# Kernel tuning notes

Measured on AMD Instinct MI355X. Metric: run time of the kernel, lower is better.

The kernel has to match this reference:

```python
import jax, jax.numpy as jnp
import numpy as np

D_MODEL = 384
D_INNER = 768   # 2 * d_model
D_STATE = 16
DT_RANK = 24    # ceil(d_model/16)
K_CONV = 4
BATCH = 8
SEQ = 2048
EPS = 1e-5


def _layer_norm(x, w, b):
    mu = x.mean(-1, keepdims=True)
    var = ((x - mu) ** 2).mean(-1, keepdims=True)
    return (x - mu) * jax.lax.rsqrt(var + EPS) * w + b


def _silu(x):
    return x * jax.nn.sigmoid(x)


def _mamba_mixer(x, in_proj, conv_w, conv_b, x_proj, dt_w, dt_b, A_log, Dp, out_proj):
    # x: (B, L, d_model)
    xz = x @ in_proj.T                      # (B, L, 2*d_inner)
    xs, z = jnp.split(xz, 2, axis=-1)       # each (B, L, d_inner)
    # causal depthwise conv1d (pad left k-1)
    xc = jnp.transpose(xs, (0, 2, 1))       # (B, d_inner, L)
    xc = jnp.pad(xc, ((0, 0), (0, 0), (K_CONV - 1, 0)))
    xc = jax.lax.conv_general_dilated(
        xc, conv_w, window_strides=(1,), padding='VALID',
        feature_group_count=D_INNER,
        dimension_numbers=('NCH', 'OIH', 'NCH'))
    xs = _silu(jnp.transpose(xc, (0, 2, 1)) + conv_b)   # (B, L, d_inner)
    # input-dependent SSM parameters
    x_dbl = xs @ x_proj.T                    # (B, L, dt_rank + 2*d_state)
    dt, Bm, Cm = jnp.split(x_dbl, [DT_RANK, DT_RANK + D_STATE], axis=-1)
    dt = jax.nn.softplus(dt @ dt_w.T + dt_b)  # (B, L, d_inner)
    A = -jnp.exp(A_log)                       # (d_inner, d_state)

    def step(h, inp):
        dt_t, B_t, C_t, x_t = inp             # (B,d), (B,N), (B,N), (B,d)
        h = jnp.exp(dt_t[:, :, None] * A) * h + (dt_t * x_t)[:, :, None] * B_t[:, None, :]
        y = jnp.einsum('bdn,bn->bd', h, C_t)
        return h, y

    h0 = jnp.zeros((xs.shape[0], D_INNER, D_STATE), xs.dtype)
    inps = (jnp.moveaxis(dt, 1, 0), jnp.moveaxis(Bm, 1, 0),
            jnp.moveaxis(Cm, 1, 0), jnp.moveaxis(xs, 1, 0))
    _, ys = jax.lax.scan(step, h0, inps)      # ys: (L, B, d_inner)
    y = jnp.moveaxis(ys, 0, 1) + xs * Dp      # skip term D*x
    y = y * _silu(z)                          # gated output
    return y @ out_proj.T                     # (B, L, d_model)


def setup_inputs() -> dict:
    key = jax.random.key(0)
    ks = jax.random.split(key, 10)
    s = 0.02
    A_init = jnp.broadcast_to(jnp.log(jnp.arange(1, D_STATE + 1, dtype=jnp.float32)),
                              (2, D_INNER, D_STATE))
    return {
        'x': jax.random.normal(ks[0], (BATCH, SEQ, D_MODEL), jnp.float32),
        'norm_w': jnp.ones((2, D_MODEL), jnp.float32),
        'norm_b': jnp.zeros((2, D_MODEL), jnp.float32),
        'in_proj': jax.random.normal(ks[1], (2, 2 * D_INNER, D_MODEL)) * s,
        'conv_w': jax.random.normal(ks[2], (2, D_INNER, 1, K_CONV)) * 0.2,
        'conv_b': jax.random.normal(ks[3], (2, D_INNER)) * s,
        'x_proj': jax.random.normal(ks[4], (2, DT_RANK + 2 * D_STATE, D_INNER)) * s,
        'dt_w': jax.random.normal(ks[5], (2, D_INNER, DT_RANK)) * s,
        'dt_b': jax.random.normal(ks[6], (2, D_INNER)) * 0.1 - 4.0,
        'A_log': A_init,
        'Dp': jnp.ones((2, D_INNER), jnp.float32),
        'out_proj': jax.random.normal(ks[7], (2, D_MODEL, D_INNER)) * s,
    }


def reference(x, norm_w, norm_b, in_proj, conv_w, conv_b, x_proj, dt_w, dt_b, A_log, Dp, out_proj):
    def blk(i, h):
        return h + _mamba_mixer(_layer_norm(h, norm_w[i], norm_b[i]),
                                in_proj[i], conv_w[i], conv_b[i], x_proj[i],
                                dt_w[i], dt_b[i], A_log[i], Dp[i], out_proj[i])
    h = blk(0, x)                    # forward-direction block
    h = jnp.flip(h, axis=-2)         # reverse sequence
    h = blk(1, h)                    # backward-direction block
    return jnp.flip(h, axis=-2)      # restore order
```

## Files before the change

### kernel.cpp

```cpp
#include <hip/hip_runtime.h>
#include <hip/hip_bf16.h>
#include <cstddef>

#define D_MODEL 384
#define D_INNER 768
#define D_STATE 16
#define DT_RANK 24
#define K_CONV  4
#define BATCH   8
#define SEQ     2048
#define BL      (BATCH * SEQ)
#define NCHUNK  32
#define LCHUNK  (SEQ / NCHUNK)
#define XDBL_LD 64

typedef unsigned short ushort_t;
typedef __bf16 bf16x8 __attribute__((ext_vector_type(8)));
typedef float  f32x4  __attribute__((ext_vector_type(4)));
typedef unsigned short u16x8 __attribute__((ext_vector_type(8)));

#define GLOBAL_AS(p) ((const __attribute__((address_space(1))) void*)(p))
#define LDS_AS(p)    ((__attribute__((address_space(3))) void*)(p))

__device__ __forceinline__ ushort_t f32_to_bf16_rne(float v) {
    unsigned int u = __float_as_uint(v);
    return (ushort_t)((u + 0x7FFFu + ((u >> 16) & 1u)) >> 16);
}
__device__ __forceinline__ float bf16_to_f32(ushort_t u) {
    return __uint_as_float(((unsigned int)u) << 16);
}

__global__ __launch_bounds__(256) void cast_bf16_kernel(
    const float* __restrict__ in, ushort_t* __restrict__ out, int n)
{
    int i = blockIdx.x * 256 + threadIdx.x;
    if (i < n) out[i] = f32_to_bf16_rne(in[i]);
}

__global__ __launch_bounds__(256) void cast_xproj_kernel(
    const float* __restrict__ in, ushort_t* __restrict__ out)
{
    int i = blockIdx.x * 256 + threadIdx.x;
    if (i >= 2 * 64 * D_INNER) return;
    int c   = i % D_INNER;
    int r   = (i / D_INNER) % 64;
    int dir = i / (64 * D_INNER);
    out[i] = (r < 56) ? f32_to_bf16_rne(in[((size_t)dir * 56 + r) * D_INNER + c])
                      : (ushort_t)0;
}

__global__ __launch_bounds__(256) void prep_transpose_kernel(
    const float* __restrict__ conv_w, const float* __restrict__ A_log,
    const float* __restrict__ dt_w, float* __restrict__ cwt,
    float* __restrict__ alt, float* __restrict__ dwt)
{
    int i = blockIdx.x * 256 + threadIdx.x;
    const int NCW = 2 * K_CONV * D_INNER;
    const int NAL = 2 * D_STATE * D_INNER;
    const int NDW = 2 * DT_RANK * D_INNER;
    if (i < NCW) {
        int c = i % D_INNER, k = (i / D_INNER) % K_CONV, dir = i / (K_CONV * D_INNER);
        cwt[i] = conv_w[((size_t)dir * D_INNER + c) * K_CONV + k];
    } else if (i < NCW + NAL) {
        int j = i - NCW;
        int d = j % D_INNER, n = (j / D_INNER) % D_STATE, dir = j / (D_STATE * D_INNER);
        alt[j] = A_log[((size_t)dir * D_INNER + d) * D_STATE + n];
    } else if (i < NCW + NAL + NDW) {
        int j = i - NCW - NAL;
        int d = j % D_INNER, r = (j / D_INNER) % DT_RANK, dir = j / (DT_RANK * D_INNER);
        dwt[j] = dt_w[((size_t)dir * D_INNER + d) * DT_RANK + r];
    }
}

__global__ __launch_bounds__(384) void ln_kernel(
    const float* __restrict__ in, const float* __restrict__ w,
    const float* __restrict__ b, ushort_t* __restrict__ out)
{
    int row = blockIdx.x;
    int tid = threadIdx.x;
    float v = in[(size_t)row * D_MODEL + tid];
    float s = v, sq = v * v;
    #pragma unroll
    for (int o = 32; o; o >>= 1) {
        s  += __shfl_down(s, o);
        sq += __shfl_down(sq, o);
    }
    __shared__ float ss[6], ssq[6];
    __shared__ float mb[2];
    int wid = tid >> 6;
    if ((tid & 63) == 0) { ss[wid] = s; ssq[wid] = sq; }
    __syncthreads();
    if (tid == 0) {
        float S = 0.f, Q = 0.f;
        #pragma unroll
        for (int k = 0; k < 6; k++) { S += ss[k]; Q += ssq[k]; }
        float mu  = S * (1.0f / D_MODEL);
        float var = Q * (1.0f / D_MODEL) - mu * mu;
        mb[0] = mu;
        mb[1] = rsqrtf(var + 1e-5f);
    }
    __syncthreads();
    float r = (v - mb[0]) * mb[1] * w[tid] + b[tid];
    out[(size_t)row * D_MODEL + tid] = f32_to_bf16_rne(r);
}

__global__ __launch_bounds__(256) void gemm_mfma_b16(
    const ushort_t* __restrict__ A, const ushort_t* __restrict__ W,
    ushort_t* __restrict__ C, int N, int K)
{
    __shared__ __bf16 As[128 * 32];
    __shared__ __bf16 Ws[128 * 32];
    int tid  = threadIdx.x;
    int bm = blockIdx.x, bn = blockIdx.y;
    int lane = tid & 63, wave = tid >> 6;
    int wr = wave >> 1, wc = wave & 1;
    int quad = lane >> 4, l16 = lane & 15;

    const ushort_t* Ag = A + (size_t)(bm * 128 + (tid >> 2)) * K + (tid & 3) * 8;
    const ushort_t* Wg = W + (size_t)(bn * 128 + (tid >> 2)) * K + (tid & 3) * 8;

    f32x4 acc[4][4] = {};

    for (int k0 = 0; k0 < K; k0 += 32) {
        __syncthreads();
        __builtin_amdgcn_global_load_lds(GLOBAL_AS(Ag + k0),
                                         LDS_AS(As + tid * 8), 16, 0, 0);
        __builtin_amdgcn_global_load_lds(GLOBAL_AS(Ag + (size_t)64 * K + k0),
                                         LDS_AS(As + 2048 + tid * 8), 16, 0, 0);
        __builtin_amdgcn_global_load_lds(GLOBAL_AS(Wg + k0),
                                         LDS_AS(Ws + tid * 8), 16, 0, 0);
        __builtin_amdgcn_global_load_lds(GLOBAL_AS(Wg + (size_t)64 * K + k0),
                                         LDS_AS(Ws + 2048 + tid * 8), 16, 0, 0);
        __syncthreads();

        bf16x8 af[4], wf[4];
        #pragma unroll
        for (int i = 0; i < 4; i++)
            af[i] = *(const bf16x8*)(As + (wr * 64 + i * 16 + l16) * 32 + quad * 8);
        #pragma unroll
        for (int j = 0; j < 4; j++)
            wf[j] = *(const bf16x8*)(Ws + (wc * 64 + j * 16 + l16) * 32 + quad * 8);
        #pragma unroll
        for (int i = 0; i < 4; i++)
            #pragma unroll
            for (int j = 0; j < 4; j++)
                acc[i][j] = __builtin_amdgcn_mfma_f32_16x16x32_bf16(
                    af[i], wf[j], acc[i][j], 0, 0, 0);
    }

    #pragma unroll
    for (int i = 0; i < 4; i++) {
        #pragma unroll
        for (int r = 0; r < 4; r++) {
            int row = bm * 128 + wr * 64 + i * 16 + quad * 4 + r;
            #pragma unroll
            for (int j = 0; j < 4; j++) {
                int col = bn * 128 + wc * 64 + j * 16 + l16;
                C[(size_t)row * N + col] = f32_to_bf16_rne(acc[i][j][r]);
            }
        }
    }
}

__global__ __launch_bounds__(256) void gemm_mfma_f32(
    const ushort_t* __restrict__ A, const ushort_t* __restrict__ W,
    const float* __restrict__ resid, float* __restrict__ C, int N, int K)
{
    __shared__ __bf16 As[128 * 32];
    __shared__ __bf16 Ws[128 * 32];
    int tid  = threadIdx.x;
    int bm = blockIdx.x, bn = blockIdx.y;
    int lane = tid & 63, wave = tid >> 6;
    int wr = wave >> 1, wc = wave & 1;
    int quad = lane >> 4, l16 = lane & 15;

    const ushort_t* Ag = A + (size_t)(bm * 128 + (tid >> 2)) * K + (tid & 3) * 8;
    const ushort_t* Wg = W + (size_t)(bn * 128 + (tid >> 2)) * K + (tid & 3) * 8;

    f32x4 acc[4][4] = {};

    for (int k0 = 0; k0 < K; k0 += 32) {
        __syncthreads();
        __builtin_amdgcn_global_load_lds(GLOBAL_AS(Ag + k0),
                                         LDS_AS(As + tid * 8), 16, 0, 0);
        __builtin_amdgcn_global_load_lds(GLOBAL_AS(Ag + (size_t)64 * K + k0),
                                         LDS_AS(As + 2048 + tid * 8), 16, 0, 0);
        __builtin_amdgcn_global_load_lds(GLOBAL_AS(Wg + k0),
                                         LDS_AS(Ws + tid * 8), 16, 0, 0);
        __builtin_amdgcn_global_load_lds(GLOBAL_AS(Wg + (size_t)64 * K + k0),
                                         LDS_AS(Ws + 2048 + tid * 8), 16, 0, 0);
        __syncthreads();

        bf16x8 af[4], wf[4];
        #pragma unroll
        for (int i = 0; i < 4; i++)
            af[i] = *(const bf16x8*)(As + (wr * 64 + i * 16 + l16) * 32 + quad * 8);
        #pragma unroll
        for (int j = 0; j < 4; j++)
            wf[j] = *(const bf16x8*)(Ws + (wc * 64 + j * 16 + l16) * 32 + quad * 8);
        #pragma unroll
        for (int i = 0; i < 4; i++)
            #pragma unroll
            for (int j = 0; j < 4; j++)
                acc[i][j] = __builtin_amdgcn_mfma_f32_16x16x32_bf16(
                    af[i], wf[j], acc[i][j], 0, 0, 0);
    }

    #pragma unroll
    for (int i = 0; i < 4; i++) {
        #pragma unroll
        for (int r = 0; r < 4; r++) {
            int row = bm * 128 + wr * 64 + i * 16 + quad * 4 + r;
            #pragma unroll
            for (int j = 0; j < 4; j++) {
                int col = bn * 128 + wc * 64 + j * 16 + l16;
                size_t idx = (size_t)row * N + col;
                C[idx] = acc[i][j][r] + resid[idx];
            }
        }
    }
}

__global__ __launch_bounds__(256) void xdbl_mfma(
    const ushort_t* __restrict__ A, const ushort_t* __restrict__ W,
    float* __restrict__ C)
{
    __shared__ __bf16 As[128 * 32];
    __shared__ __bf16 Ws[64 * 32];
    int tid  = threadIdx.x;
    int bm = blockIdx.x;
    int lane = tid & 63, wave = tid >> 6;
    int quad = lane >> 4, l16 = lane & 15;

    const ushort_t* Ag = A + (size_t)(bm * 128 + (tid >> 2)) * D_INNER + (tid & 3) * 8;
    const ushort_t* Wg = W + (size_t)(tid >> 2) * D_INNER + (tid & 3) * 8;

    f32x4 acc[2][4] = {};

    for (int k0 = 0; k0 < D_INNER; k0 += 32) {
        __syncthreads();
        __builtin_amdgcn_global_load_lds(GLOBAL_AS(Ag + k0),
                                         LDS_AS(As + tid * 8), 16, 0, 0);
        __builtin_amdgcn_global_load_lds(GLOBAL_AS(Ag + (size_t)64 * D_INNER + k0),
                                         LDS_AS(As + 2048 + tid * 8), 16, 0, 0);
        __builtin_amdgcn_global_load_lds(GLOBAL_AS(Wg + k0),
                                         LDS_AS(Ws + tid * 8), 16, 0, 0);
        __syncthreads();

        bf16x8 af[2], wf[4];
        #pragma unroll
        for (int i = 0; i < 2; i++)
            af[i] = *(const bf16x8*)(As + (wave * 32 + i * 16 + l16) * 32 + quad * 8);
        #pragma unroll
        for (int j = 0; j < 4; j++)
            wf[j] = *(const bf16x8*)(Ws + (j * 16 + l16) * 32 + quad * 8);
        #pragma unroll
        for (int i = 0; i < 2; i++)
            #pragma unroll
            for (int j = 0; j < 4; j++)
                acc[i][j] = __builtin_amdgcn_mfma_f32_16x16x32_bf16(
                    af[i], wf[j], acc[i][j], 0, 0, 0);
    }

    #pragma unroll
    for (int i = 0; i < 2; i++) {
        #pragma unroll
        for (int r = 0; r < 4; r++) {
            int row = bm * 128 + wave * 32 + i * 16 + quad * 4 + r;
            #pragma unroll
            for (int j = 0; j < 4; j++) {
                int col = j * 16 + l16;
                C[(size_t)row * XDBL_LD + col] = acc[i][j][r];
            }
        }
    }
}

__global__ __launch_bounds__(256) void conv_silu_kernel(
    const ushort_t* __restrict__ xz, const float* __restrict__ cwt,
    const float* __restrict__ cb, ushort_t* __restrict__ xsc, int dir)
{
    int idx8 = blockIdx.x * 256 + threadIdx.x;
    int c8   = (idx8 % 96) * 8;
    int row  = idx8 / 96;
    int l    = row % SEQ;
    int b0   = row - l;

    float acc[8];
    float4 bv0 = *(const float4*)(cb + c8);
    float4 bv1 = *(const float4*)(cb + c8 + 4);
    acc[0] = bv0.x; acc[1] = bv0.y; acc[2] = bv0.z; acc[3] = bv0.w;
    acc[4] = bv1.x; acc[5] = bv1.y; acc[6] = bv1.z; acc[7] = bv1.w;

    #pragma unroll
    for (int k = 0; k < 4; k++) {
        int ls = dir ? (l + k) : (l - 3 + k);
        int wk = dir ? (3 - k) : k;
        bool ok = dir ? (ls < SEQ) : (ls >= 0);
        if (ok) {
            u16x8 v = *(const u16x8*)(xz + (size_t)(b0 + ls) * 1536 + c8);
            float4 w0 = *(const float4*)(cwt + wk * D_INNER + c8);
            float4 w1 = *(const float4*)(cwt + wk * D_INNER + c8 + 4);
            float wv[8] = {w0.x, w0.y, w0.z, w0.w, w1.x, w1.y, w1.z, w1.w};
            #pragma unroll
            for (int j = 0; j < 8; j++)
                acc[j] = fmaf(bf16_to_f32(v[j]), wv[j], acc[j]);
        }
    }
    u16x8 o;
    #pragma unroll
    for (int j = 0; j < 8; j++) {
        float sg = 1.0f / (1.0f + __expf(-acc[j]));
        o[j] = f32_to_bf16_rne(acc[j] * sg);
    }
    *(u16x8*)(xsc + (size_t)row * D_INNER + c8) = o;
}

__global__ __launch_bounds__(256) void scan_pass1(
    const ushort_t* __restrict__ xsc, const float* __restrict__ xdbl,
    const float* __restrict__ dwt, const float* __restrict__ dtbias,
    const float* __restrict__ alt,
    float* __restrict__ hstate, float* __restrict__ sumdt_buf, int dir)
{
    int g = blockIdx.x % 3;
    int c = (blockIdx.x / 3) % NCHUNK;
    int b = blockIdx.x / (3 * NCHUNK);
    int d = g * 256 + threadIdx.x;
    float A[D_STATE], w[DT_RANK];
    #pragma unroll
    for (int n = 0; n < D_STATE; n++) A[n] = -__expf(alt[n * D_INNER + d]);
    #pragma unroll
    for (int r = 0; r < DT_RANK; r++) w[r] = dwt[r * D_INNER + d];
    float bias = dtbias[d];
    float h[D_STATE] = {};
    float sdt = 0.f;
    size_t base = (size_t)b * SEQ;
    for (int i = 0; i < LCHUNK; i++) {
        int p = c * LCHUNK + i;
        int l = dir ? (SEQ - 1 - p) : p;
        size_t row = base + l;
        const float* xr = xdbl + row * XDBL_LD;
        float acc = bias;
        #pragma unroll
        for (int r = 0; r < DT_RANK; r++) acc = fmaf(xr[r], w[r], acc);
        float dtv = acc > 20.f ? acc : __logf(1.f + __expf(acc));
        float xv  = bf16_to_f32(xsc[row * D_INNER + d]);
        float dtx = dtv * xv;
        sdt += dtv;
        const float* Br = xr + DT_RANK;
        #pragma unroll
        for (int n = 0; n < D_STATE; n++)
            h[n] = fmaf(__expf(dtv * A[n]), h[n], dtx * Br[n]);
    }
    size_t cidx = (size_t)(b * NCHUNK + c) * D_INNER + d;
    sumdt_buf[cidx] = sdt;
    #pragma unroll
    for (int n = 0; n < D_STATE; n++) hstate[cidx * D_STATE + n] = h[n];
}

__global__ __launch_bounds__(256) void scan_pass2(
    float* __restrict__ hstate, const float* __restrict__ sumdt_buf,
    const float* __restrict__ alt)
{
    int gid = blockIdx.x * 256 + threadIdx.x;
    int n = gid & 15;
    int d = (gid >> 4) % D_INNER;
    int b = gid / (16 * D_INNER);
    float A = -__expf(alt[n * D_INNER + d]);
    float h = 0.f;
    for (int c = 0; c < NCHUNK; c++) {
        size_t cidx = (size_t)(b * NCHUNK + c) * D_INNER + d;
        float ho = hstate[cidx * D_STATE + n];
        hstate[cidx * D_STATE + n] = h;
        h = fmaf(__expf(A * sumdt_buf[cidx]), h, ho);
    }
}

__global__ __launch_bounds__(256) void scan_pass3(
    const ushort_t* __restrict__ xsc, const ushort_t* __restrict__ xz,
    const float* __restrict__ xdbl, const float* __restrict__ dwt,
    const float* __restrict__ dtbias, const float* __restrict__ alt,
    const float* __restrict__ Dp, const float* __restrict__ hstate,
    ushort_t* __restrict__ y, int dir)
{
    int g = blockIdx.x % 3;
    int c = (blockIdx.x / 3) % NCHUNK;
    int b = blockIdx.x / (3 * NCHUNK);
    int d = g * 256 + threadIdx.x;
    size_t cidx = (size_t)(b * NCHUNK + c) * D_INNER + d;
    float A[D_STATE], h[D_STATE], w[DT_RANK];
    #pragma unroll
    for (int n = 0; n < D_STATE; n++) {
        A[n] = -__expf(alt[n * D_INNER + d]);
        h[n] = hstate[cidx * D_STATE + n];
    }
    #pragma unroll
    for (int r = 0; r < DT_RANK; r++) w[r] = dwt[r * D_INNER + d];
    float bias = dtbias[d];
    float Dd = Dp[d];
    size_t base = (size_t)b * SEQ;
    for (int i = 0; i < LCHUNK; i++) {
        int p = c * LCHUNK + i;
        int l = dir ? (SEQ - 1 - p) : p;
        size_t row = base + l;
        const float* xr = xdbl + row * XDBL_LD;
        float acc = bias;
        #pragma unroll
        for (int r = 0; r < DT_RANK; r++) acc = fmaf(xr[r], w[r], acc);
        float dtv = acc > 20.f ? acc : __logf(1.f + __expf(acc));
        float xv  = bf16_to_f32(xsc[row * D_INNER + d]);
        float zv  = bf16_to_f32(xz[row * 1536 + D_INNER + d]);
        float dtx = dtv * xv;
        const float* Br = xr + DT_RANK;
        const float* Cr = xr + DT_RANK + D_STATE;
        float yv = 0.f;
        #pragma unroll
        for (int n = 0; n < D_STATE; n++) {
            h[n] = fmaf(__expf(dtv * A[n]), h[n], dtx * Br[n]);
            yv = fmaf(h[n], Cr[n], yv);
        }
        yv = fmaf(xv, Dd, yv);
        float sg = 1.f / (1.f + __expf(-zv));
        yv *= zv * sg;
        y[row * D_INNER + d] = f32_to_bf16_rne(yv);
    }
}

extern "C" void kernel_launch(void* const* d_in, const int* in_sizes, int n_in,
                              void* d_out, int out_size, void* d_ws, size_t ws_size,
                              hipStream_t stream)
{
    const float* x       = (const float*)d_in[0];
    const float* norm_w  = (const float*)d_in[1];
    const float* norm_b  = (const float*)d_in[2];
    const float* in_proj = (const float*)d_in[3];
    const float* conv_w  = (const float*)d_in[4];
    const float* conv_b  = (const float*)d_in[5];
    const float* x_proj  = (const float*)d_in[6];
    const float* dt_w    = (const float*)d_in[7];
    const float* dt_b    = (const float*)d_in[8];
    const float* A_log   = (const float*)d_in[9];
    const float* Dp      = (const float*)d_in[10];
    const float* out_proj= (const float*)d_in[11];
    float* out = (float*)d_out;

    float* ws   = (float*)d_ws;
    float* reg0 = ws;                ws += (size_t)BL * D_INNER / 2;
    ushort_t* lnb = (ushort_t*)reg0;
    ushort_t* ybf = (ushort_t*)reg0;
    ushort_t* xzb  = (ushort_t*)ws;  ws += (size_t)BL * 1536 / 2;
    ushort_t* xscb = (ushort_t*)ws;  ws += (size_t)BL * D_INNER / 2;
    float* xdbl = ws;                ws += (size_t)BL * XDBL_LD;
    float* sumdt  = ws;              ws += (size_t)BATCH * NCHUNK * D_INNER;
    float* hstate = ws;              ws += (size_t)BATCH * NCHUNK * D_INNER * D_STATE;
    ushort_t* wbf_in  = (ushort_t*)ws;  ws += (size_t)2 * 1536 * D_MODEL / 2;
    ushort_t* wbf_out = (ushort_t*)ws;  ws += (size_t)2 * D_MODEL * D_INNER / 2;
    ushort_t* xp_bf   = (ushort_t*)ws;  ws += (size_t)2 * 64 * D_INNER / 2;
    float* cwt = ws;                 ws += (size_t)2 * K_CONV * D_INNER;
    float* alt = ws;                 ws += (size_t)2 * D_STATE * D_INNER;
    float* dwt = ws;                 ws += (size_t)2 * DT_RANK * D_INNER;

    cast_bf16_kernel<<<(2 * 1536 * D_MODEL + 255) / 256, 256, 0, stream>>>(
        in_proj, wbf_in, 2 * 1536 * D_MODEL);
    cast_bf16_kernel<<<(2 * D_MODEL * D_INNER + 255) / 256, 256, 0, stream>>>(
        out_proj, wbf_out, 2 * D_MODEL * D_INNER);
    cast_xproj_kernel<<<(2 * 64 * D_INNER + 255) / 256, 256, 0, stream>>>(
        x_proj, xp_bf);
    {
        int total = 2 * (K_CONV + D_STATE + DT_RANK) * D_INNER;
        prep_transpose_kernel<<<(total + 255) / 256, 256, 0, stream>>>(
            conv_w, A_log, dt_w, cwt, alt, dwt);
    }

    for (int i = 0; i < 2; i++) {
        const float* hinp = (i == 0) ? x : out;
        ln_kernel<<<BL, 384, 0, stream>>>(hinp, norm_w + i * D_MODEL,
                                          norm_b + i * D_MODEL, lnb);
        gemm_mfma_b16<<<dim3(BL / 128, 1536 / 128), 256, 0, stream>>>(
            lnb, wbf_in + (size_t)i * 1536 * D_MODEL, xzb, 1536, D_MODEL);
        conv_silu_kernel<<<(BL * 96) / 256, 256, 0, stream>>>(
            xzb, cwt + (size_t)i * K_CONV * D_INNER, conv_b + i * D_INNER,
            xscb, i);
        xdbl_mfma<<<BL / 128, 256, 0, stream>>>(
            xscb, xp_bf + (size_t)i * 64 * D_INNER, xdbl);
        scan_pass1<<<BATCH * NCHUNK * 3, 256, 0, stream>>>(
            xscb, xdbl, dwt + (size_t)i * DT_RANK * D_INNER,
            dt_b + i * D_INNER, alt + (size_t)i * D_STATE * D_INNER,
            hstate, sumdt, i);
        scan_pass2<<<(BATCH * D_INNER * D_STATE) / 256, 256, 0, stream>>>(
            hstate, sumdt, alt + (size_t)i * D_STATE * D_INNER);
        scan_pass3<<<BATCH * NCHUNK * 3, 256, 0, stream>>>(
            xscb, xzb, xdbl, dwt + (size_t)i * DT_RANK * D_INNER,
            dt_b + i * D_INNER, alt + (size_t)i * D_STATE * D_INNER,
            Dp + i * D_INNER, hstate, ybf, i);
        gemm_mfma_f32<<<dim3(BL / 128, D_MODEL / 128), 256, 0, stream>>>(
            ybf, wbf_out + (size_t)i * D_MODEL * D_INNER, hinp, out,
            D_MODEL, D_INNER);
    }
}
```

Baseline: 594.0 us.

## Precompute dt in separate kernel, double scan chunks, use exp2 with prescaled A

Moves the dt projection and softplus out of both scan passes into a new dt_kernel that writes dt as bf16, so the delta computation runs once instead of twice per direction. Doubles NCHUNK to 64 so the scan passes launch more blocks, and replaces __expf with hardware exp2 by prescaling A with log2(e). The cost is an extra kernel launch, an extra bf16 buffer of BL*D_INNER written and read twice, reduced dt precision from storing it as bf16, and a longer sequential loop in pass2.

Result: faster. 545.7 us (-8.1%).

```diff
diff --git a/kernel.cpp b/kernel.cpp
--- a/kernel.cpp
+++ b/kernel.cpp
@@ -10,9 +10,10 @@
 #define BATCH   8
 #define SEQ     2048
 #define BL      (BATCH * SEQ)
-#define NCHUNK  32
+#define NCHUNK  64
 #define LCHUNK  (SEQ / NCHUNK)
 #define XDBL_LD 64
+#define LOG2E   1.44269504088896f
 
 typedef unsigned short ushort_t;
 typedef __bf16 bf16x8 __attribute__((ext_vector_type(8)));
@@ -276,6 +277,34 @@
     }
 }
 
+__global__ __launch_bounds__(256) void dt_kernel(
+    const float* __restrict__ xdbl, const float* __restrict__ dwt,
+    const float* __restrict__ dtbias, ushort_t* __restrict__ dtb)
+{
+    int g    = blockIdx.x % 3;
+    int row0 = (blockIdx.x / 3) * 16;
+    int tid  = threadIdx.x;
+    int d    = g * 256 + tid;
+    float w[DT_RANK];
+    #pragma unroll
+    for (int r = 0; r < DT_RANK; r++) w[r] = dwt[r * D_INNER + d];
+    float bias = dtbias[d];
+    __shared__ float xd[16][DT_RANK];
+    if (tid < 16 * DT_RANK) {
+        int rr = tid / DT_RANK, cc = tid % DT_RANK;
+        xd[rr][cc] = xdbl[(size_t)(row0 + rr) * XDBL_LD + cc];
+    }
+    __syncthreads();
+    #pragma unroll 4
+    for (int i = 0; i < 16; i++) {
+        float acc = bias;
+        #pragma unroll
+        for (int r = 0; r < DT_RANK; r++) acc = fmaf(xd[i][r], w[r], acc);
+        float sp = acc > 20.f ? acc : __logf(1.f + __expf(acc));
+        dtb[(size_t)(row0 + i) * D_INNER + d] = f32_to_bf16_rne(sp);
+    }
+}
+
 __global__ __launch_bounds__(256) void conv_silu_kernel(
     const ushort_t* __restrict__ xz, const float* __restrict__ cwt,
     const float* __restrict__ cb, ushort_t* __restrict__ xsc, int dir)
@@ -317,21 +346,18 @@
 }
 
 __global__ __launch_bounds__(256) void scan_pass1(
-    const ushort_t* __restrict__ xsc, const float* __restrict__ xdbl,
-    const float* __restrict__ dwt, const float* __restrict__ dtbias,
-    const float* __restrict__ alt,
+    const ushort_t* __restrict__ xsc, const ushort_t* __restrict__ dtb,
+    const float* __restrict__ xdbl, const float* __restrict__ alt,
     float* __restrict__ hstate, float* __restrict__ sumdt_buf, int dir)
 {
     int g = blockIdx.x % 3;
     int c = (blockIdx.x / 3) % NCHUNK;
     int b = blockIdx.x / (3 * NCHUNK);
     int d = g * 256 + threadIdx.x;
-    float A[D_STATE], w[DT_RANK];
-    #pragma unroll
-    for (int n = 0; n < D_STATE; n++) A[n] = -__expf(alt[n * D_INNER + d]);
-    #pragma unroll
-    for (int r = 0; r < DT_RANK; r++) w[r] = dwt[r * D_INNER + d];
-    float bias = dtbias[d];
+    float A2[D_STATE];
+    #pragma unroll
+    for (int n = 0; n < D_STATE; n++)
+        A2[n] = -__expf(alt[n * D_INNER + d]) * LOG2E;
     float h[D_STATE] = {};
     float sdt = 0.f;
     size_t base = (size_t)b * SEQ;
@@ -339,18 +365,14 @@
         int p = c * LCHUNK + i;
         int l = dir ? (SEQ - 1 - p) : p;
         size_t row = base + l;
-        const float* xr = xdbl + row * XDBL_LD;
-        float acc = bias;
-        #pragma unroll
-        for (int r = 0; r < DT_RANK; r++) acc = fmaf(xr[r], w[r], acc);
-        float dtv = acc > 20.f ? acc : __logf(1.f + __expf(acc));
+        float dtv = bf16_to_f32(dtb[row * D_INNER + d]);
         float xv  = bf16_to_f32(xsc[row * D_INNER + d]);
         float dtx = dtv * xv;
         sdt += dtv;
-        const float* Br = xr + DT_RANK;
+        const float* Br = xdbl + row * XDBL_LD + DT_RANK;
         #pragma unroll
         for (int n = 0; n < D_STATE; n++)
-            h[n] = fmaf(__expf(dtv * A[n]), h[n], dtx * Br[n]);
+            h[n] = fmaf(__builtin_amdgcn_exp2f(dtv * A2[n]), h[n], dtx * Br[n]);
     }
     size_t cidx = (size_t)(b * NCHUNK + c) * D_INNER + d;
     sumdt_buf[cidx] = sdt;
@@ -366,57 +388,49 @@
     int n = gid & 15;
     int d = (gid >> 4) % D_INNER;
     int b = gid / (16 * D_INNER);
-    float A = -__expf(alt[n * D_INNER + d]);
+    float A2 = -__expf(alt[n * D_INNER + d]) * LOG2E;
     float h = 0.f;
     for (int c = 0; c < NCHUNK; c++) {
         size_t cidx = (size_t)(b * NCHUNK + c) * D_INNER + d;
         float ho = hstate[cidx * D_STATE + n];
         hstate[cidx * D_STATE + n] = h;
-        h = fmaf(__expf(A * sumdt_buf[cidx]), h, ho);
+        h = fmaf(__builtin_amdgcn_exp2f(A2 * sumdt_buf[cidx]), h, ho);
     }
 }
 
 __global__ __launch_bounds__(256) void scan_pass3(
-    const ushort_t* __restrict__ xsc, const ushort_t* __restrict__ xz,
-    const float* __restrict__ xdbl, const float* __restrict__ dwt,
-    const float* __restrict__ dtbias, const float* __restrict__ alt,
-    const float* __restrict__ Dp, const float* __restrict__ hstate,
-    ushort_t* __restrict__ y, int dir)
+    const ushort_t* __restrict__ xsc, const ushort_t* __restrict__ dtb,
+    const ushort_t* __restrict__ xz, const float* __restrict__ xdbl,
+    const float* __restrict__ alt, const float* __restrict__ Dp,
+    const float* __restrict__ hstate, ushort_t* __restrict__ y, int dir)
 {
     int g = blockIdx.x % 3;
     int c = (blockIdx.x / 3) % NCHUNK;
     int b = blockIdx.x / (3 * NCHUNK);
     int d = g * 256 + threadIdx.x;
     size_t cidx = (size_t)(b * NCHUNK + c) * D_INNER + d;
-    float A[D_STATE], h[D_STATE], w[DT_RANK];
+    float A2[D_STATE], h[D_STATE];
     #pragma unroll
     for (int n = 0; n < D_STATE; n++) {
-        A[n] = -__expf(alt[n * D_INNER + d]);
+        A2[n] = -__expf(alt[n * D_INNER + d]) * LOG2E;
         h[n] = hstate[cidx * D_STATE + n];
     }
-    #pragma unroll
-    for (int r = 0; r < DT_RANK; r++) w[r] = dwt[r * D_INNER + d];
-    float bias = dtbias[d];
     float Dd = Dp[d];
     size_t base = (size_t)b * SEQ;
     for (int i = 0; i < LCHUNK; i++) {
         int p = c * LCHUNK + i;
         int l = dir ? (SEQ - 1 - p) : p;
         size_t row = base + l;
-        const float* xr = xdbl + row * XDBL_LD;
-        float acc = bias;
-        #pragma unroll
-        for (int r = 0; r < DT_RANK; r++) acc = fmaf(xr[r], w[r], acc);
-        float dtv = acc > 20.f ? acc : __logf(1.f + __expf(acc));
+        float dtv = bf16_to_f32(dtb[row * D_INNER + d]);
         float xv  = bf16_to_f32(xsc[row * D_INNER + d]);
         float zv  = bf16_to_f32(xz[row * 1536 + D_INNER + d]);
         float dtx = dtv * xv;
-        const float* Br = xr + DT_RANK;
-        const float* Cr = xr + DT_RANK + D_STATE;
+        const float* Br = xdbl + row * XDBL_LD + DT_RANK;
+        const float* Cr = xdbl + row * XDBL_LD + DT_RANK + D_STATE;
         float yv = 0.f;
         #pragma unroll
         for (int n = 0; n < D_STATE; n++) {
-            h[n] = fmaf(__expf(dtv * A[n]), h[n], dtx * Br[n]);
+            h[n] = fmaf(__builtin_amdgcn_exp2f(dtv * A2[n]), h[n], dtx * Br[n]);
             yv = fmaf(h[n], Cr[n], yv);
         }
         yv = fmaf(xv, Dd, yv);
@@ -450,6 +464,7 @@
     ushort_t* ybf = (ushort_t*)reg0;
     ushort_t* xzb  = (ushort_t*)ws;  ws += (size_t)BL * 1536 / 2;
     ushort_t* xscb = (ushort_t*)ws;  ws += (size_t)BL * D_INNER / 2;
+    ushort_t* dtb  = (ushort_t*)ws;  ws += (size_t)BL * D_INNER / 2;
     float* xdbl = ws;                ws += (size_t)BL * XDBL_LD;
     float* sumdt  = ws;              ws += (size_t)BATCH * NCHUNK * D_INNER;
     float* hstate = ws;              ws += (size_t)BATCH * NCHUNK * D_INNER * D_STATE;
@@ -483,15 +498,15 @@
             xscb, i);
         xdbl_mfma<<<BL / 128, 256, 0, stream>>>(
             xscb, xp_bf + (size_t)i * 64 * D_INNER, xdbl);
+        dt_kernel<<<(BL / 16) * 3, 256, 0, stream>>>(
+            xdbl, dwt + (size_t)i * DT_RANK * D_INNER, dt_b + i * D_INNER, dtb);
         scan_pass1<<<BATCH * NCHUNK * 3, 256, 0, stream>>>(
-            xscb, xdbl, dwt + (size_t)i * DT_RANK * D_INNER,
-            dt_b + i * D_INNER, alt + (size_t)i * D_STATE * D_INNER,
+            xscb, dtb, xdbl, alt + (size_t)i * D_STATE * D_INNER,
             hstate, sumdt, i);
         scan_pass2<<<(BATCH * D_INNER * D_STATE) / 256, 256, 0, stream>>>(
             hstate, sumdt, alt + (size_t)i * D_STATE * D_INNER);
         scan_pass3<<<BATCH * NCHUNK * 3, 256, 0, stream>>>(
-            xscb, xzb, xdbl, dwt + (size_t)i * DT_RANK * D_INNER,
-            dt_b + i * D_INNER, alt + (size_t)i * D_STATE * D_INNER,
+            xscb, dtb, xzb, xdbl, alt + (size_t)i * D_STATE * D_INNER,
             Dp + i * D_INNER, hstate, ybf, i);
         gemm_mfma_f32<<<dim3(BL / 128, D_MODEL / 128), 256, 0, stream>>>(
             ybf, wbf_out + (size_t)i * D_MODEL * D_INNER, hinp, out,
```
